# Kernel optimization log

Hardware: AMD Instinct MI355X
Metric: run time of the kernel (lower is better)

The kernel has to match this reference:

```python
import jax, jax.numpy as jnp
import numpy as np

TARGET_H, TARGET_W = 602, 602
EPS = 1e-8
A = -0.75  # PyTorch bicubic kernel coefficient


def _cubic_kernel(x):
    # Keys cubic convolution kernel with a = -0.75 (PyTorch's choice), x >= 0
    x = np.abs(x)
    w = np.where(
        x <= 1.0,
        (A + 2.0) * x**3 - (A + 3.0) * x**2 + 1.0,
        np.where(x < 2.0, A * (x**3 - 5.0 * x**2 + 8.0 * x - 4.0), 0.0),
    )
    return w


def build_bicubic_matrix(in_size, out_size):
    # Row-stochastic [out_size, in_size] matrix equivalent to 1D bicubic resize
    # with align_corners=False and border replication (PyTorch F.interpolate).
    scale = in_size / out_size
    i = np.arange(out_size, dtype=np.float64)
    src = (i + 0.5) * scale - 0.5
    base = np.floor(src).astype(np.int64)
    t = src - base
    W = np.zeros((out_size, in_size), dtype=np.float64)
    for tap in range(-1, 3):
        idx = np.clip(base + tap, 0, in_size - 1)
        w = _cubic_kernel(t - tap)
        np.add.at(W, (np.arange(out_size), idx), w)
    return jnp.asarray(W, dtype=jnp.float32)


def setup_inputs() -> dict:
    key = jax.random.key(0)
    k1, k2 = jax.random.split(key)
    B, K, D, N = 4, 1849, 1024, 80
    feats = jax.random.normal(k1, (B, K, D), dtype=jnp.float32)
    embeddings = jax.random.normal(k2, (N, D), dtype=jnp.float32)
    return {"feats": feats, "embeddings": embeddings}


def reference(feats, embeddings) -> jnp.ndarray:
    B, K, D = feats.shape
    N = embeddings.shape[0]
    P = int(np.sqrt(K))  # patch grid side (43)

    # Cosine similarity ('init' branch with normalize=True), expressed as a GEMM
    dot = jnp.einsum("bkd,nd->bnk", feats, embeddings)  # [B,N,K]
    f_norm = jnp.linalg.norm(feats, axis=-1)       # [B,K]
    e_norm = jnp.linalg.norm(embeddings, axis=-1)  # [N]
    cosim = dot / (f_norm[:, None, :] * e_norm[None, :, None] + EPS)

    cosim = cosim.reshape(B, N, P, P)

    # Separable bicubic resize to (TARGET_H, TARGET_W)
    Wh = build_bicubic_matrix(P, TARGET_H)  # [602, P]
    Ww = build_bicubic_matrix(P, TARGET_W)  # [602, P]
    out = jnp.einsum("bnhw,Hh->bnHw", cosim, Wh)
    out = jnp.einsum("bnHw,Ww->bnHW", out, Ww)
    return out
```

## Files before the change

### kernel.cpp

```cpp
#include <hip/hip_runtime.h>
#include <math.h>

#define EPS 1e-8f
constexpr int D     = 1024;
constexpr int NEMB  = 80;
constexpr int K     = 1849;
constexpr int BATCH = 4;
constexpr int P     = 43;
constexpr int TGT   = 602;
constexpr int ROWS  = BATCH * K;
constexpr size_t PLANE = (size_t)BATCH * NEMB * K;
constexpr int SPLIT = 8;
constexpr int KC    = D / SPLIT;

typedef float nfloat4 __attribute__((ext_vector_type(4)));

__device__ inline double cubic_w(double x) {
  const double A = -0.75;
  x = fabs(x);
  if (x <= 1.0) return ((A + 2.0) * x - (A + 3.0)) * x * x + 1.0;
  if (x < 2.0)  return A * (((x - 5.0) * x + 8.0) * x - 4.0);
  return 0.0;
}

__device__ inline float block_reduce_sum256(float v) {
  #pragma unroll
  for (int off = 32; off > 0; off >>= 1) v += __shfl_down(v, off, 64);
  __shared__ float red[4];
  int lane = threadIdx.x & 63, wid = threadIdx.x >> 6;
  if (lane == 0) red[wid] = v;
  __syncthreads();
  float r = 0.f;
  if (threadIdx.x == 0) r = red[0] + red[1] + red[2] + red[3];
  return r;
}

__global__ __launch_bounds__(256) void prep_kernel(
    const float* __restrict__ emb, float* __restrict__ e_norm,
    float4* __restrict__ gtw) {
  int bid = blockIdx.x;
  if (bid < NEMB) {
    float4 v = ((const float4*)(emb + (size_t)bid * D))[threadIdx.x];
    float s = v.x * v.x + v.y * v.y + v.z * v.z + v.w * v.w;
    s = block_reduce_sum256(s);
    if (threadIdx.x == 0) e_norm[bid] = sqrtf(s);
  } else {
    int j = threadIdx.x;
    if (j < 14) {
      double scale = (double)P / (double)TGT;
      double src = ((double)j + 0.5) * scale - 0.5;
      double fb = floor(src);
      double t = src - fb;
      float4 w;
      w.x = (float)cubic_w(t + 1.0);
      w.y = (float)cubic_w(t);
      w.z = (float)cubic_w(t - 1.0);
      w.w = (float)cubic_w(t - 2.0);
      gtw[j] = w;
    }
  }
}

constexpr int BM  = 64;
constexpr int BK  = 32;
constexpr int LDA = 36;
constexpr int NT  = KC / BK;

__device__ inline float dot4(float4 v) {
  return v.x * v.x + v.y * v.y + v.z * v.z + v.w * v.w;
}

__global__ __launch_bounds__(256) void gemm_partial(
    const float* __restrict__ feats, const float* __restrict__ emb,
    float* __restrict__ part, float* __restrict__ fpart) {
  __shared__ float As[BM * LDA];
  __shared__ float Bs[NEMB * LDA];
  int t = threadIdx.x;
  int row0 = blockIdx.x * BM;
  int s = blockIdx.y;
  int tr = t >> 4, tc = t & 15;
  float acc[4][5] = {{0.f}};
  float ssq0 = 0.f, ssq1 = 0.f;

  int r = t >> 3, dg = t & 7;
  int gr0 = row0 + r, gr1 = row0 + 32 + r;
  bool ok0 = gr0 < ROWS, ok1 = gr1 < ROWS;
  const float* pA0 = feats + (size_t)gr0 * D + dg * 4;
  const float* pA1 = feats + (size_t)gr1 * D + dg * 4;
  const float* pB0 = emb + (size_t)r * D + dg * 4;
  const float* pB1 = emb + (size_t)(32 + r) * D + dg * 4;
  const float* pB2 = emb + (size_t)(64 + r) * D + dg * 4;
  bool okB2 = t < 128;

  int kbeg = s * KC;
  const float4 zero = make_float4(0.f, 0.f, 0.f, 0.f);
  float4 a0 = ok0 ? *(const float4*)(pA0 + kbeg) : zero;
  float4 a1 = ok1 ? *(const float4*)(pA1 + kbeg) : zero;
  float4 b0 = *(const float4*)(pB0 + kbeg);
  float4 b1 = *(const float4*)(pB1 + kbeg);
  float4 b2 = okB2 ? *(const float4*)(pB2 + kbeg) : zero;

  for (int tile = 0; tile < NT; ++tile) {
    ssq0 += dot4(a0);
    *(float4*)(As + r * LDA + dg * 4) = a0;
    ssq1 += dot4(a1);
    *(float4*)(As + (32 + r) * LDA + dg * 4) = a1;
    *(float4*)(Bs + r * LDA + dg * 4) = b0;
    *(float4*)(Bs + (32 + r) * LDA + dg * 4) = b1;
    if (okB2) *(float4*)(Bs + (64 + r) * LDA + dg * 4) = b2;
    __syncthreads();

    if (tile + 1 < NT) {
      int k1 = kbeg + (tile + 1) * BK;
      a0 = ok0 ? *(const float4*)(pA0 + k1) : zero;
      a1 = ok1 ? *(const float4*)(pA1 + k1) : zero;
      b0 = *(const float4*)(pB0 + k1);
      b1 = *(const float4*)(pB1 + k1);
      if (okB2) b2 = *(const float4*)(pB2 + k1);
    }

    #pragma unroll
    for (int dd = 0; dd < BK; dd += 4) {
      float4 a[4], b[5];
      #pragma unroll
      for (int j = 0; j < 4; ++j)  a[j]  = *(const float4*)(As + (tr * 4 + j) * LDA + dd);
      #pragma unroll
      for (int i2 = 0; i2 < 5; ++i2) b[i2] = *(const float4*)(Bs + (tc + i2 * 16) * LDA + dd);
      #pragma unroll
      for (int j = 0; j < 4; ++j)
        #pragma unroll
        for (int i2 = 0; i2 < 5; ++i2)
          acc[j][i2] += a[j].x * b[i2].x + a[j].y * b[i2].y +
                        a[j].z * b[i2].z + a[j].w * b[i2].w;
    }
    __syncthreads();
  }

  #pragma unroll
  for (int off = 4; off > 0; off >>= 1) {
    ssq0 += __shfl_down(ssq0, off, 8);
    ssq1 += __shfl_down(ssq1, off, 8);
  }
  if ((t & 7) == 0) {
    if (gr0 < ROWS) fpart[(size_t)s * ROWS + gr0] = ssq0;
    if (gr1 < ROWS) fpart[(size_t)s * ROWS + gr1] = ssq1;
  }

  float* pplane = part + (size_t)s * PLANE;
  #pragma unroll
  for (int j = 0; j < 4; ++j) {
    int gr = row0 + tr * 4 + j;
    if (gr >= ROWS) continue;
    int b_ = gr / K;
    int k  = gr - b_ * K;
    #pragma unroll
    for (int i2 = 0; i2 < 5; ++i2) {
      int n = tc + i2 * 16;
      pplane[((size_t)(b_ * NEMB + n)) * K + k] = acc[j][i2];
    }
  }
}

__global__ __launch_bounds__(256) void reduce_kernel(
    const float* __restrict__ part, const float* __restrict__ fpart,
    const float* __restrict__ e_norm, float* __restrict__ cosim) {
  size_t e = (size_t)blockIdx.x * 256 + threadIdx.x;
  if (e >= PLANE) return;
  int bn = (int)(e / K);
  int k  = (int)(e - (size_t)bn * K);
  int b_ = bn / NEMB;
  int n  = bn - b_ * NEMB;
  int gr = b_ * K + k;
  float dot = 0.f, fn2 = 0.f;
  #pragma unroll
  for (int s = 0; s < SPLIT; ++s) {
    dot += part[(size_t)s * PLANE + e];
    fn2 += fpart[(size_t)s * ROWS + gr];
  }
  cosim[e] = dot / (sqrtf(fn2) * e_norm[n] + EPS);
}

__global__ __launch_bounds__(320) void resize_kernel(
    const float* __restrict__ cosim, const float4* __restrict__ gtw,
    float* __restrict__ out) {
  __shared__ float img[5 * P];
  __shared__ float4 wq[14];
  __shared__ float obuf[14 * TGT];

  int bn = blockIdx.y;
  int c  = blockIdx.x;
  int t  = threadIdx.x;

  int hmin = max(0, c - 2), hmax = min(P - 1, c + 2);
  int NH = hmax - hmin + 1;

  if (t < 14) wq[t] = gtw[t];
  const float* src = cosim + (size_t)bn * (P * P) + hmin * P;
  for (int i = t; i < NH * P; i += 320) img[i] = src[i];
  __syncthreads();

  int pw = t;
  if (pw < TGT / 2) {
    int W0 = pw * 2;
    int m0 = W0 / 14;
    int j0 = W0 - m0 * 14;
    int wb0 = m0 - 2 + (j0 >= 7);
    int j1 = (j0 == 13) ? 0 : j0 + 1;
    int d  = (j0 == 6) ? 1 : 0;
    float4 w0 = wq[j0], w1 = wq[j1];

    int i0 = min(P - 1, max(0, wb0));
    int i1 = min(P - 1, max(0, wb0 + 1));
    int i2 = min(P - 1, max(0, wb0 + 2));
    int i3 = min(P - 1, max(0, wb0 + 3));
    int i4 = min(P - 1, max(0, wb0 + 4));

    float ta[5], tb[5];
    #pragma unroll
    for (int h = 0; h < 5; ++h) {
      const float* rowp = img + h * P;
      float v0 = rowp[i0], v1 = rowp[i1], v2 = rowp[i2], v3 = rowp[i3], v4 = rowp[i4];
      ta[h] = w0.x * v0 + w0.y * v1 + w0.z * v2 + w0.w * v3;
      float u0 = d ? v1 : v0;
      float u1 = d ? v2 : v1;
      float u2 = d ? v3 : v2;
      float u3 = d ? v4 : v3;
      tb[h] = w1.x * u0 + w1.y * u1 + w1.z * u2 + w1.w * u3;
    }

    #define ROWS7(R0, a0, a1, a2, a3)                                        \
      _Pragma("unroll")                                                      \
      for (int r = R0; r < R0 + 7; ++r) {                                    \
        float4 hw = wq[r];                                                   \
        float ox = hw.x * ta[a0] + hw.y * ta[a1] + hw.z * ta[a2] + hw.w * ta[a3]; \
        float oy = hw.x * tb[a0] + hw.y * tb[a1] + hw.z * tb[a2] + hw.w * tb[a3]; \
        *(float2*)(obuf + r * TGT + W0) = make_float2(ox, oy);               \
      }

    if (c >= 2 && c <= 40) {
      ROWS7(0, 0, 1, 2, 3)
      ROWS7(7, 1, 2, 3, 4)
    } else if (c == 0) {
      ROWS7(0, 0, 0, 0, 1)
      ROWS7(7, 0, 0, 1, 2)
    } else if (c == 1) {
      ROWS7(0, 0, 0, 1, 2)
      ROWS7(7, 0, 1, 2, 3)
    } else if (c == 41) {
      ROWS7(0, 0, 1, 2, 3)
      ROWS7(7, 1, 2, 3, 3)
    } else {
      ROWS7(0, 0, 1, 2, 2)
      ROWS7(7, 1, 2, 2, 2)
    }
    #undef ROWS7
  }
  __syncthreads();

  nfloat4* dst = (nfloat4*)(out + (size_t)bn * TGT * TGT + (size_t)c * 14 * TGT);
  const nfloat4* sb = (const nfloat4*)obuf;
  constexpr int NVEC = 14 * TGT / 4;
  for (int i = t; i < NVEC; i += 320) {
    __builtin_nontemporal_store(sb[i], dst + i);
  }
}

extern "C" void kernel_launch(void* const* d_in, const int* in_sizes, int n_in,
                              void* d_out, int out_size, void* d_ws, size_t ws_size,
                              hipStream_t stream) {
  const float* feats = (const float*)d_in[0];
  const float* emb   = (const float*)d_in[1];
  float* out = (float*)d_out;
  char* ws = (char*)d_ws;

  auto align64 = [](size_t x) { return (x + 63) & ~(size_t)63; };
  size_t off = 0;
  float* cosim  = (float*)(ws + off); off = align64(off + PLANE * 4);
  float* e_norm = (float*)(ws + off); off = align64(off + NEMB * 4);
  float4* gtw   = (float4*)(ws + off); off = align64(off + 14 * 16);

  float* fpart = (float*)(ws + off); off = align64(off + (size_t)SPLIT * ROWS * 4);
  float* part  = (float*)(ws + off); off = align64(off + (size_t)SPLIT * PLANE * 4);

  prep_kernel<<<dim3(NEMB + 1), dim3(256), 0, stream>>>(emb, e_norm, gtw);
  gemm_partial<<<dim3((ROWS + BM - 1) / BM, SPLIT), dim3(256), 0, stream>>>(
      feats, emb, part, fpart);
  reduce_kernel<<<dim3((int)((PLANE + 255) / 256)), dim3(256), 0, stream>>>(
      part, fpart, e_norm, cosim);
  resize_kernel<<<dim3(43, 320), dim3(320), 0, stream>>>(cosim, gtw, out);
}
```

Baseline: 175.6 us.

## Make resize kernel persistent with register-prefetched next chunk input

Replaces the 43x320 block grid of the bicubic resize with a persistent grid of 1024 blocks that loop over chunks. Each iteration prefetches the next chunk's 5-row input slice into a register while computing and storing the current one. The aim is to cut block launch and setup overhead and hide global load latency. In exchange it adds extra barriers per iteration and may lower the number of in-flight stores compared with a fully oversubscribed grid.

```diff
diff --git a/kernel.cpp b/kernel.cpp
--- a/kernel.cpp
+++ b/kernel.cpp
@@ -180,6 +180,9 @@
   cosim[e] = dot / (sqrtf(fn2) * e_norm[n] + EPS);
 }
 
+constexpr int NCHUNK = 320 * 43;
+constexpr int RGRID  = 1024;
+
 __global__ __launch_bounds__(320) void resize_kernel(
     const float* __restrict__ cosim, const float4* __restrict__ gtw,
     float* __restrict__ out) {
@@ -187,81 +190,94 @@
   __shared__ float4 wq[14];
   __shared__ float obuf[14 * TGT];
 
-  int bn = blockIdx.y;
-  int c  = blockIdx.x;
-  int t  = threadIdx.x;
-
-  int hmin = max(0, c - 2), hmax = min(P - 1, c + 2);
-  int NH = hmax - hmin + 1;
-
+  int t = threadIdx.x;
   if (t < 14) wq[t] = gtw[t];
-  const float* src = cosim + (size_t)bn * (P * P) + hmin * P;
-  for (int i = t; i < NH * P; i += 320) img[i] = src[i];
-  __syncthreads();
-
-  int pw = t;
-  if (pw < TGT / 2) {
-    int W0 = pw * 2;
-    int m0 = W0 / 14;
-    int j0 = W0 - m0 * 14;
-    int wb0 = m0 - 2 + (j0 >= 7);
-    int j1 = (j0 == 13) ? 0 : j0 + 1;
-    int d  = (j0 == 6) ? 1 : 0;
-    float4 w0 = wq[j0], w1 = wq[j1];
-
-    int i0 = min(P - 1, max(0, wb0));
-    int i1 = min(P - 1, max(0, wb0 + 1));
-    int i2 = min(P - 1, max(0, wb0 + 2));
-    int i3 = min(P - 1, max(0, wb0 + 3));
-    int i4 = min(P - 1, max(0, wb0 + 4));
-
-    float ta[5], tb[5];
-    #pragma unroll
-    for (int h = 0; h < 5; ++h) {
-      const float* rowp = img + h * P;
-      float v0 = rowp[i0], v1 = rowp[i1], v2 = rowp[i2], v3 = rowp[i3], v4 = rowp[i4];
-      ta[h] = w0.x * v0 + w0.y * v1 + w0.z * v2 + w0.w * v3;
-      float u0 = d ? v1 : v0;
-      float u1 = d ? v2 : v1;
-      float u2 = d ? v3 : v2;
-      float u3 = d ? v4 : v3;
-      tb[h] = w1.x * u0 + w1.y * u1 + w1.z * u2 + w1.w * u3;
-    }
-
-    #define ROWS7(R0, a0, a1, a2, a3)                                        \
-      _Pragma("unroll")                                                      \
-      for (int r = R0; r < R0 + 7; ++r) {                                    \
-        float4 hw = wq[r];                                                   \
-        float ox = hw.x * ta[a0] + hw.y * ta[a1] + hw.z * ta[a2] + hw.w * ta[a3]; \
-        float oy = hw.x * tb[a0] + hw.y * tb[a1] + hw.z * tb[a2] + hw.w * tb[a3]; \
-        *(float2*)(obuf + r * TGT + W0) = make_float2(ox, oy);               \
+
+  int hrel = t / P, col = t - hrel * P;
+  auto img_load = [&](int cid) -> float {
+    if (t >= 5 * P) return 0.f;
+    int bn = cid / 43, c = cid - (cid / 43) * 43;
+    int hmin = max(0, c - 2);
+    int row = min(P - 1, hmin + hrel);
+    return cosim[(size_t)bn * (P * P) + row * P + col];
+  };
+
+  int cid = blockIdx.x;
+  float v = (cid < NCHUNK) ? img_load(cid) : 0.f;
+
+  while (cid < NCHUNK) {
+    int next = cid + RGRID;
+    __syncthreads();
+    if (t < 5 * P) img[t] = v;
+    if (next < NCHUNK) v = img_load(next);
+    __syncthreads();
+
+    int bn = cid / 43, c = cid - (cid / 43) * 43;
+
+    if (t < TGT / 2) {
+      int W0 = t * 2;
+      int m0 = W0 / 14;
+      int j0 = W0 - m0 * 14;
+      int wb0 = m0 - 2 + (j0 >= 7);
+      int j1 = (j0 == 13) ? 0 : j0 + 1;
+      int d  = (j0 == 6) ? 1 : 0;
+      float4 w0 = wq[j0], w1 = wq[j1];
+
+      int i0 = min(P - 1, max(0, wb0));
+      int i1 = min(P - 1, max(0, wb0 + 1));
+      int i2 = min(P - 1, max(0, wb0 + 2));
+      int i3 = min(P - 1, max(0, wb0 + 3));
+      int i4 = min(P - 1, max(0, wb0 + 4));
+
+      float ta[5], tb[5];
+      #pragma unroll
+      for (int h = 0; h < 5; ++h) {
+        const float* rowp = img + h * P;
+        float v0 = rowp[i0], v1 = rowp[i1], v2 = rowp[i2], v3 = rowp[i3], v4 = rowp[i4];
+        ta[h] = w0.x * v0 + w0.y * v1 + w0.z * v2 + w0.w * v3;
+        float u0 = d ? v1 : v0;
+        float u1 = d ? v2 : v1;
+        float u2 = d ? v3 : v2;
+        float u3 = d ? v4 : v3;
+        tb[h] = w1.x * u0 + w1.y * u1 + w1.z * u2 + w1.w * u3;
       }
 
-    if (c >= 2 && c <= 40) {
-      ROWS7(0, 0, 1, 2, 3)
-      ROWS7(7, 1, 2, 3, 4)
-    } else if (c == 0) {
-      ROWS7(0, 0, 0, 0, 1)
-      ROWS7(7, 0, 0, 1, 2)
-    } else if (c == 1) {
-      ROWS7(0, 0, 0, 1, 2)
-      ROWS7(7, 0, 1, 2, 3)
-    } else if (c == 41) {
-      ROWS7(0, 0, 1, 2, 3)
-      ROWS7(7, 1, 2, 3, 3)
-    } else {
-      ROWS7(0, 0, 1, 2, 2)
-      ROWS7(7, 1, 2, 2, 2)
-    }
-    #undef ROWS7
-  }
-  __syncthreads();
-
-  nfloat4* dst = (nfloat4*)(out + (size_t)bn * TGT * TGT + (size_t)c * 14 * TGT);
-  const nfloat4* sb = (const nfloat4*)obuf;
-  constexpr int NVEC = 14 * TGT / 4;
-  for (int i = t; i < NVEC; i += 320) {
-    __builtin_nontemporal_store(sb[i], dst + i);
+      #define ROWS7(R0, a0, a1, a2, a3)                                        \
+        _Pragma("unroll")                                                      \
+        for (int r = R0; r < R0 + 7; ++r) {                                    \
+          float4 hw = wq[r];                                                   \
+          float ox = hw.x * ta[a0] + hw.y * ta[a1] + hw.z * ta[a2] + hw.w * ta[a3]; \
+          float oy = hw.x * tb[a0] + hw.y * tb[a1] + hw.z * tb[a2] + hw.w * tb[a3]; \
+          *(float2*)(obuf + r * TGT + W0) = make_float2(ox, oy);               \
+        }
+
+      if (c >= 2 && c <= 40) {
+        ROWS7(0, 0, 1, 2, 3)
+        ROWS7(7, 1, 2, 3, 4)
+      } else if (c == 0) {
+        ROWS7(0, 0, 0, 0, 1)
+        ROWS7(7, 0, 0, 1, 2)
+      } else if (c == 1) {
+        ROWS7(0, 0, 0, 1, 2)
+        ROWS7(7, 0, 1, 2, 3)
+      } else if (c == 41) {
+        ROWS7(0, 0, 1, 2, 3)
+        ROWS7(7, 1, 2, 3, 3)
+      } else {
+        ROWS7(0, 0, 1, 2, 2)
+        ROWS7(7, 1, 2, 2, 2)
+      }
+      #undef ROWS7
+    }
+    __syncthreads();
+
+    nfloat4* dst = (nfloat4*)(out + (size_t)bn * TGT * TGT + (size_t)c * 14 * TGT);
+    const nfloat4* sb = (const nfloat4*)obuf;
+    constexpr int NVEC = 14 * TGT / 4;
+    for (int i = t; i < NVEC; i += 320) {
+      __builtin_nontemporal_store(sb[i], dst + i);
+    }
+    cid = next;
   }
 }
 
@@ -287,5 +303,5 @@
       feats, emb, part, fpart);
   reduce_kernel<<<dim3((int)((PLANE + 255) / 256)), dim3(256), 0, stream>>>(
       part, fpart, e_norm, cosim);
-  resize_kernel<<<dim3(43, 320), dim3(320), 0, stream>>>(cosim, gtw, out);
-}
+  resize_kernel<<<dim3(RGRID), dim3(320), 0, stream>>>(cosim, gtw, out);
+}
```

After: 191.0 us. 8.8% more time.
